# Performance work log

Measured on AMD Instinct MI355X. Metric: run time of the kernel, lower is better.

Reference implementation:

```python
import jax, jax.numpy as jnp
import numpy as np

B, T, D, K = 16, 4096, 128, 1024
BETA = 0.25


def setup_inputs() -> dict:
    key = jax.random.key(0)
    k1, k2 = jax.random.split(key)
    z_e = jax.random.normal(k1, (B, T, D), dtype=jnp.float32)
    # tf.random.uniform default: U[0, 1)
    vecs_embedding = jax.random.uniform(k2, (K, D), dtype=jnp.float32)
    return {"z_e": z_e, "vecs_embedding": vecs_embedding}


def reference(z_e, vecs_embedding):
    # dot_z_embedding: [B, T, K]
    dot = jnp.einsum('btd,kd->btk', z_e, vecs_embedding)
    norm_sq_z = jnp.sum(jnp.square(z_e), axis=-1)              # [B, T]
    norm_sq_e = jnp.sum(jnp.square(vecs_embedding), axis=-1)   # [K]
    dist = -2.0 * dot + norm_sq_z[..., None] + norm_sq_e       # [B, T, K]
    ids = jnp.argmin(dist, axis=-1)                            # [B, T]
    z_q = vecs_embedding[ids]                                  # [B, T, D]
    # tf.norm over channel axis (axes[0] == 2), then mean over batch*time
    loss_commit = jnp.mean(jnp.linalg.norm(jax.lax.stop_gradient(z_e) - z_q, axis=-1))
    loss_codebook = jnp.mean(jnp.linalg.norm(z_e - jax.lax.stop_gradient(z_q), axis=-1))
    loss = loss_codebook + BETA * loss_commit
    similarity = dot / jnp.sqrt(norm_sq_z)[..., None] / jnp.sqrt(norm_sq_e)
    return z_q, similarity, ids, loss
```

## Files before the change

### kernel.cpp

```cpp
#include <hip/hip_runtime.h>
#include <math.h>

#define MTOT 65536
#define DD   128
#define KK   1024
#define BETA 0.25f
#define TM   64
#define NCH  64

typedef __attribute__((ext_vector_type(8))) short short8;
typedef __attribute__((ext_vector_type(4))) float float4v;

__device__ __forceinline__ unsigned bf16_rne(float x) {
    unsigned u = __float_as_uint(x);
    return (u + 0x7fffu + ((u >> 16) & 1u)) >> 16;
}

__device__ __forceinline__ void gload_lds16(const void* g, void* l) {
    __builtin_amdgcn_global_load_lds(
        (const __attribute__((address_space(1))) unsigned int*)g,
        (__attribute__((address_space(3))) unsigned int*)l, 16, 0, 0);
}

__global__ void k_norms(const float* __restrict__ e, ushort* __restrict__ bp,
                        float* __restrict__ nef, float* __restrict__ inef,
                        float* __restrict__ loss) {
    const int gw = blockIdx.x * 4 + (threadIdx.x >> 6);
    const int lane = threadIdx.x & 63;
    char* hb = (char*)bp;
    char* lb = hb + 262144;
    const int sub = lane & 3;
    for (int code = gw; code < KK; code += 256) {
        float2 ev = ((const float2*)(e + (size_t)code * DD))[lane];
        unsigned h0 = bf16_rne(ev.x), h1 = bf16_rne(ev.y);
        float l0f = ev.x - __uint_as_float(h0 << 16);
        float l1f = ev.y - __uint_as_float(h1 << 16);
        ushort2 hv; hv.x = (ushort)h0; hv.y = (ushort)h1;
        ushort2 lv; lv.x = (ushort)bf16_rne(l0f); lv.y = (ushort)bf16_rne(l1f);
        int sw = (((lane >> 2) * 16) ^ ((code & 7) << 4)) + sub * 4;
        *(ushort2*)(hb + code * 256 + sw) = hv;
        *(ushort2*)(lb + code * 256 + sw) = lv;
        float s = ev.x * ev.x + ev.y * ev.y;
        #pragma unroll
        for (int off = 32; off; off >>= 1) s += __shfl_down(s, off, 64);
        if (lane == 0) { nef[code] = s; inef[code] = 1.0f / sqrtf(s); }
    }
    if (blockIdx.x == 0 && threadIdx.x == 0) *loss = 0.0f;
}

__device__ __forceinline__ void merge2(float& v1, int& i1, float& v2, int& i2,
                                       float ov1, int oi1, float ov2, int oi2) {
    bool l1 = (ov1 < v1) || (ov1 == v1 && oi1 < i1);
    if (l1) {
        bool l2 = (ov2 < v1) || (ov2 == v1 && oi2 < i1);
        v2 = l2 ? ov2 : v1; i2 = l2 ? oi2 : i1;
        v1 = ov1; i1 = oi1;
    } else {
        bool l2 = (ov1 < v2) || (ov1 == v2 && oi1 < i2);
        if (l2) { v2 = ov1; i2 = oi1; }
    }
}

__launch_bounds__(256, 2)
__global__ void k_main(const float* __restrict__ z, float* __restrict__ sim,
                       const ushort* __restrict__ bpre,
                       const float* __restrict__ nef, const float* __restrict__ inef,
                       const float* __restrict__ e, float* __restrict__ zq,
                       float* __restrict__ idsf, float* __restrict__ loss) {
    __shared__ __align__(16) ushort Bs[2 * 16384];
    __shared__ unsigned candL[TM];
    __shared__ float bs[4];

    const int t = threadIdx.x;
    const int w = t >> 6, lane = t & 63, cl = lane & 15, q = lane >> 4;
    const int mh = (w & 1) * 32, nh = (w >> 1) * 32;
    const int r0 = blockIdx.x * TM;

    auto STAGE = [&](int buf, int ch2) {
        const char* gb = (const char*)bpre + (size_t)ch2 * 16384;
        #pragma unroll
        for (int i = 0; i < 8; ++i) {
            int slot = i * 256 + t;
            int goff = slot * 16 + ((slot >= 1024) ? 245760 : 0);
            gload_lds16(gb + goff,
                        (char*)Bs + buf * 32768 + (i * 256 + (t & 0xFFC0)) * 16);
        }
    };

    STAGE(0, 0);

    short8 afh[2][4], afl[2][4];
    float pn0 = 0.0f, pn1 = 0.0f;
    const char* zb = (const char*)z;
    #pragma unroll
    for (int mt = 0; mt < 2; ++mt) {
        const char* rp = zb + (size_t)(r0 + mh + mt * 16 + cl) * 512;
        #pragma unroll
        for (int s = 0; s < 4; ++s) {
            float4v f0 = *(const float4v*)(rp + s * 128 + q * 32);
            float4v f1 = *(const float4v*)(rp + s * 128 + q * 32 + 16);
            short8 h, l;
            float ps = 0.0f;
            #pragma unroll
            for (int j = 0; j < 4; ++j) {
                float fx = f0[j];
                unsigned hu = bf16_rne(fx);
                h[j] = (short)hu;
                l[j] = (short)bf16_rne(fx - __uint_as_float(hu << 16));
                ps += fx * fx;
                float fy = f1[j];
                unsigned hw2 = bf16_rne(fy);
                h[j + 4] = (short)hw2;
                l[j + 4] = (short)bf16_rne(fy - __uint_as_float(hw2 << 16));
                ps += fy * fy;
            }
            afh[mt][s] = h; afl[mt][s] = l;
            if (mt == 0) pn0 += ps; else pn1 += ps;
        }
    }
    pn0 += __shfl_xor(pn0, 16, 64); pn0 += __shfl_xor(pn0, 32, 64);
    pn1 += __shfl_xor(pn1, 16, 64); pn1 += __shfl_xor(pn1, 32, 64);
    float inzr[2]; inzr[0] = 1.0f / sqrtf(pn0); inzr[1] = 1.0f / sqrtf(pn1);
    __syncthreads();

    float b1v[2], b2v[2]; int b1i[2], b2i[2];
    #pragma unroll
    for (int s = 0; s < 2; ++s) { b1v[s] = 3.4e38f; b2v[s] = 3.4e38f; b1i[s] = 0; b2i[s] = 0; }

    const int swz = (cl & 7) << 4;
    for (int ch = 0; ch < 16; ++ch) {
        const int c0 = ch * NCH;
        const char* Bb = (const char*)Bs + (ch & 1) * 32768;
        if (ch < 15) STAGE((ch + 1) & 1, ch + 1);

        float4v ne4[2], ine4[2];
        #pragma unroll
        for (int ct = 0; ct < 2; ++ct) {
            int cb = c0 + nh + ct * 16 + q * 4;
            ne4[ct]  = *(const float4v*)(nef + cb);
            ine4[ct] = *(const float4v*)(inef + cb);
        }

        float4v acc[2][2];
        #pragma unroll
        for (int ct = 0; ct < 2; ++ct)
            #pragma unroll
            for (int zt = 0; zt < 2; ++zt) acc[ct][zt] = (float4v)(0.0f);

        short8 bh0[4], bh1[4];
        #pragma unroll
        for (int s = 0; s < 4; ++s) {
            const int ko = (s * 64 + q * 16) ^ swz;
            bh0[s] = *(const short8*)(Bb + (nh + cl) * 256 + ko);
            bh1[s] = *(const short8*)(Bb + (nh + 16 + cl) * 256 + ko);
            acc[0][0] = __builtin_amdgcn_mfma_f32_16x16x32_bf16(bh0[s], afh[0][s], acc[0][0], 0, 0, 0);
            acc[0][1] = __builtin_amdgcn_mfma_f32_16x16x32_bf16(bh0[s], afh[1][s], acc[0][1], 0, 0, 0);
            acc[1][0] = __builtin_amdgcn_mfma_f32_16x16x32_bf16(bh1[s], afh[0][s], acc[1][0], 0, 0, 0);
            acc[1][1] = __builtin_amdgcn_mfma_f32_16x16x32_bf16(bh1[s], afh[1][s], acc[1][1], 0, 0, 0);
        }
        #pragma unroll
        for (int s = 0; s < 4; ++s) {
            const int ko = (s * 64 + q * 16) ^ swz;
            short8 bl0 = *(const short8*)(Bb + 16384 + (nh + cl) * 256 + ko);
            short8 bl1 = *(const short8*)(Bb + 16384 + (nh + 16 + cl) * 256 + ko);
            acc[0][0] = __builtin_amdgcn_mfma_f32_16x16x32_bf16(bl0, afh[0][s], acc[0][0], 0, 0, 0);
            acc[0][1] = __builtin_amdgcn_mfma_f32_16x16x32_bf16(bl0, afh[1][s], acc[0][1], 0, 0, 0);
            acc[1][0] = __builtin_amdgcn_mfma_f32_16x16x32_bf16(bl1, afh[0][s], acc[1][0], 0, 0, 0);
            acc[1][1] = __builtin_amdgcn_mfma_f32_16x16x32_bf16(bl1, afh[1][s], acc[1][1], 0, 0, 0);
        }
        #pragma unroll
        for (int s = 0; s < 4; ++s) {
            acc[0][0] = __builtin_amdgcn_mfma_f32_16x16x32_bf16(bh0[s], afl[0][s], acc[0][0], 0, 0, 0);
            acc[0][1] = __builtin_amdgcn_mfma_f32_16x16x32_bf16(bh0[s], afl[1][s], acc[0][1], 0, 0, 0);
            acc[1][0] = __builtin_amdgcn_mfma_f32_16x16x32_bf16(bh1[s], afl[0][s], acc[1][0], 0, 0, 0);
            acc[1][1] = __builtin_amdgcn_mfma_f32_16x16x32_bf16(bh1[s], afl[1][s], acc[1][1], 0, 0, 0);
        }

        __syncthreads();

        #pragma unroll
        for (int zt = 0; zt < 2; ++zt) {
            const float inz = inzr[zt];
            const size_t rowg = (size_t)(r0 + mh + zt * 16 + cl);
            #pragma unroll
            for (int ct = 0; ct < 2; ++ct) {
                const int cb = c0 + nh + ct * 16 + q * 4;
                float4v d = acc[ct][zt];
                float4v sv;
                #pragma unroll
                for (int j = 0; j < 4; ++j) sv[j] = d[j] * inz * ine4[ct][j];
                *(float4v*)(sim + rowg * KK + cb) = sv;
                #pragma unroll
                for (int j = 0; j < 4; ++j) {
                    float dist = fmaf(-2.0f, d[j], ne4[ct][j]);
                    int col = cb + j;
                    if (dist < b1v[zt]) {
                        b2v[zt] = b1v[zt]; b2i[zt] = b1i[zt];
                        b1v[zt] = dist;    b1i[zt] = col;
                    } else if (dist < b2v[zt]) {
                        b2v[zt] = dist; b2i[zt] = col;
                    }
                }
            }
        }
    }

    #pragma unroll
    for (int zt = 0; zt < 2; ++zt) {
        #pragma unroll
        for (int off = 16; off <= 32; off <<= 1) {
            float ov1 = __shfl_xor(b1v[zt], off, 64);
            int   oi1 = __shfl_xor(b1i[zt], off, 64);
            float ov2 = __shfl_xor(b2v[zt], off, 64);
            int   oi2 = __shfl_xor(b2i[zt], off, 64);
            merge2(b1v[zt], b1i[zt], b2v[zt], b2i[zt], ov1, oi1, ov2, oi2);
        }
    }
    float* top = (float*)Bs;
    if (q == 0) {
        #pragma unroll
        for (int zt = 0; zt < 2; ++zt) {
            int row = mh + zt * 16 + cl;
            float4v v;
            v[0] = b1v[zt]; v[1] = __int_as_float(b1i[zt]);
            v[2] = b2v[zt]; v[3] = __int_as_float(b2i[zt]);
            *(float4v*)(top + (row * 2 + (w >> 1)) * 4) = v;
        }
    }
    __syncthreads();
    if (t < TM) {
        float4v e0 = *(const float4v*)(top + (t * 2 + 0) * 4);
        float4v e1 = *(const float4v*)(top + (t * 2 + 1) * 4);
        float v1 = e0[0], v2 = e0[2];
        int   i1 = __float_as_int(e0[1]), i2 = __float_as_int(e0[3]);
        merge2(v1, i1, v2, i2, e1[0], __float_as_int(e1[1]), e1[2], __float_as_int(e1[3]));
        candL[t] = (unsigned)i1 | ((unsigned)i2 << 16);
    }
    __syncthreads();

    float wsum = 0.0f;
    const int rloc = w * 16;
    for (int i = 0; i < 16; ++i) {
        int row = r0 + rloc + i;
        unsigned pk = candL[rloc + i];
        int c1 = (int)(pk & 0xffffu), c2 = (int)(pk >> 16);
        float2 zv = ((const float2*)(z + (size_t)row * DD))[lane];
        float2 e1 = ((const float2*)(e + (size_t)c1 * DD))[lane];
        float2 e2 = ((const float2*)(e + (size_t)c2 * DD))[lane];
        float v0 = zv.x * zv.x + zv.y * zv.y;
        float v1 = zv.x * e1.x + zv.y * e1.y;
        float v2 = zv.x * e2.x + zv.y * e2.y;
        float v3 = e1.x * e1.x + e1.y * e1.y;
        float v4 = e2.x * e2.x + e2.y * e2.y;
        #pragma unroll
        for (int off = 32; off; off >>= 1) {
            v0 += __shfl_down(v0, off, 64);
            v1 += __shfl_down(v1, off, 64);
            v2 += __shfl_down(v2, off, 64);
            v3 += __shfl_down(v3, off, 64);
            v4 += __shfl_down(v4, off, 64);
        }
        int choice = 0; float ssq = 0.0f;
        if (lane == 0) {
            float d1 = fmaf(-2.0f, v1, v0 + v3);
            float d2 = fmaf(-2.0f, v2, v0 + v4);
            choice = (d2 < d1 || (d2 == d1 && c2 < c1)) ? 1 : 0;
            ssq = choice ? d2 : d1;
        }
        choice = __shfl(choice, 0, 64);
        float2 es; es.x = choice ? e2.x : e1.x; es.y = choice ? e2.y : e1.y;
        int cs = choice ? c2 : c1;
        ((float2*)(zq + (size_t)row * DD))[lane] = es;
        if (lane == 0) {
            wsum += sqrtf(fmaxf(ssq, 0.0f));
            idsf[row] = (float)cs;
        }
    }
    if (lane == 0) bs[w] = wsum;
    __syncthreads();
    if (t == 0)
        atomicAdd(loss, (bs[0] + bs[1] + bs[2] + bs[3]) * ((1.0f + BETA) / (float)MTOT));
}

extern "C" void kernel_launch(void* const* d_in, const int* in_sizes, int n_in,
                              void* d_out, int out_size, void* d_ws, size_t ws_size,
                              hipStream_t stream) {
    const float* z = (const float*)d_in[0];
    const float* e = (const float*)d_in[1];
    float* out  = (float*)d_out;
    float* zq   = out;
    float* sim  = out + (size_t)MTOT * DD;
    float* idsf = sim + (size_t)MTOT * KK;
    float* loss = idsf + MTOT;

    ushort* bpre = (ushort*)d_ws;
    float*  nef  = (float*)((char*)d_ws + 524288);
    float*  inef = nef + 1024;

    k_norms<<<64,        256, 0, stream>>>(e, bpre, nef, inef, loss);
    k_main <<<MTOT / TM, 256, 0, stream>>>(z, sim, bpre, nef, inef, e, zq, idsf, loss);
}
```

Before: 491.2 us.

## Transpose similarity tile through LDS for coalesced stores and cache norms in LDS

Similarity outputs now pass through a per-wave swizzled LDS scratch, so each lane writes a contiguous 64-byte row segment instead of the scattered MFMA-layout float4 stores. Codebook norms and inverse norms are loaded once into LDS rather than read from global memory every chunk. The per-chunk __syncthreads is replaced by a partial vmcnt wait plus a raw barrier at the end of the iteration, intended to let global stores overlap with the next stage. The scratch round-trip has no wave barrier and relies on in-order LDS access within a wave. The extra LDS use may reduce occupancy.

```diff
diff --git a/kernel.cpp b/kernel.cpp
--- a/kernel.cpp
+++ b/kernel.cpp
@@ -68,8 +68,8 @@
                        const float* __restrict__ e, float* __restrict__ zq,
                        float* __restrict__ idsf, float* __restrict__ loss) {
     __shared__ __align__(16) ushort Bs[2 * 16384];
-    __shared__ unsigned candL[TM];
-    __shared__ float bs[4];
+    __shared__ __align__(16) float neLf[2048];
+    __shared__ __align__(16) float scr[1024];
 
     const int t = threadIdx.x;
     const int w = t >> 6, lane = t & 63, cl = lane & 15, q = lane >> 4;
@@ -86,6 +86,9 @@
                         (char*)Bs + buf * 32768 + (i * 256 + (t & 0xFFC0)) * 16);
         }
     };
+
+    *(float4v*)&neLf[t * 4]        = *(const float4v*)&nef[t * 4];
+    *(float4v*)&neLf[1024 + t * 4] = *(const float4v*)&inef[t * 4];
 
     STAGE(0, 0);
 
@@ -128,18 +131,16 @@
     for (int s = 0; s < 2; ++s) { b1v[s] = 3.4e38f; b2v[s] = 3.4e38f; b1i[s] = 0; b2i[s] = 0; }
 
     const int swz = (cl & 7) << 4;
+    float* sw = scr + w * 256;
+    const int wchunk = cl * 4 + (q ^ (cl & 3));
+    const int rrow = lane >> 2, rj = lane & 3;
+    const int rchunk = rrow * 4 + (rj ^ (rrow & 3));
+
     for (int ch = 0; ch < 16; ++ch) {
         const int c0 = ch * NCH;
         const char* Bb = (const char*)Bs + (ch & 1) * 32768;
         if (ch < 15) STAGE((ch + 1) & 1, ch + 1);
-
-        float4v ne4[2], ine4[2];
-        #pragma unroll
-        for (int ct = 0; ct < 2; ++ct) {
-            int cb = c0 + nh + ct * 16 + q * 4;
-            ne4[ct]  = *(const float4v*)(nef + cb);
-            ine4[ct] = *(const float4v*)(inef + cb);
-        }
+        __builtin_amdgcn_sched_barrier(0);
 
         float4v acc[2][2];
         #pragma unroll
@@ -176,12 +177,16 @@
             acc[1][1] = __builtin_amdgcn_mfma_f32_16x16x32_bf16(bh1[s], afl[1][s], acc[1][1], 0, 0, 0);
         }
 
-        __syncthreads();
-
+        float4v ne4[2], ine4[2];
+        #pragma unroll
+        for (int ct = 0; ct < 2; ++ct) {
+            int cb = c0 + nh + ct * 16 + q * 4;
+            ne4[ct]  = *(const float4v*)&neLf[cb];
+            ine4[ct] = *(const float4v*)&neLf[1024 + cb];
+        }
         #pragma unroll
         for (int zt = 0; zt < 2; ++zt) {
             const float inz = inzr[zt];
-            const size_t rowg = (size_t)(r0 + mh + zt * 16 + cl);
             #pragma unroll
             for (int ct = 0; ct < 2; ++ct) {
                 const int cb = c0 + nh + ct * 16 + q * 4;
@@ -189,7 +194,10 @@
                 float4v sv;
                 #pragma unroll
                 for (int j = 0; j < 4; ++j) sv[j] = d[j] * inz * ine4[ct][j];
-                *(float4v*)(sim + rowg * KK + cb) = sv;
+                *(float4v*)(sw + wchunk * 4) = sv;
+                float4v ov = *(const float4v*)(sw + rchunk * 4);
+                *(float4v*)(sim + (size_t)(r0 + mh + zt * 16 + rrow) * KK
+                                + (c0 + nh + ct * 16 + rj * 4)) = ov;
                 #pragma unroll
                 for (int j = 0; j < 4; ++j) {
                     float dist = fmaf(-2.0f, d[j], ne4[ct][j]);
@@ -203,6 +211,10 @@
                 }
             }
         }
+
+        asm volatile("s_waitcnt vmcnt(4)" ::: "memory");
+        __builtin_amdgcn_s_barrier();
+        __builtin_amdgcn_sched_barrier(0);
     }
 
     #pragma unroll
@@ -228,6 +240,8 @@
         }
     }
     __syncthreads();
+    unsigned* candL = (unsigned*)scr;
+    float* bsum = scr + 64;
     if (t < TM) {
         float4v e0 = *(const float4v*)(top + (t * 2 + 0) * 4);
         float4v e1 = *(const float4v*)(top + (t * 2 + 1) * 4);
@@ -276,10 +290,10 @@
             idsf[row] = (float)cs;
         }
     }
-    if (lane == 0) bs[w] = wsum;
+    if (lane == 0) bsum[w] = wsum;
     __syncthreads();
     if (t == 0)
-        atomicAdd(loss, (bs[0] + bs[1] + bs[2] + bs[3]) * ((1.0f + BETA) / (float)MTOT));
+        atomicAdd(loss, (bsum[0] + bsum[1] + bsum[2] + bsum[3]) * ((1.0f + BETA) / (float)MTOT));
 }
 
 extern "C" void kernel_launch(void* const* d_in, const int* in_sizes, int n_in,
```

After: 411.3 us. 16.3% less time.
